# Kernel tuning notes

Measured on AMD Instinct MI355X. Metric: run time of the kernel, lower is better.

## Reference

```python
import jax, jax.numpy as jnp
import numpy as np
import math

B, S, D = 2, 2048, 2048
H, KV, HD = 32, 8, 64
G = H // KV  # 4
BASE = 10000.0


def _rope_tables(seq_len, dtype):
    inv_freq = 1.0 / (BASE ** (jnp.arange(0, HD, 2, dtype=jnp.float32) / HD))
    t = jnp.arange(seq_len, dtype=jnp.float32)
    freqs = jnp.outer(t, inv_freq)               # [S, HD/2]
    emb = jnp.concatenate([freqs, freqs], -1)     # [S, HD]
    return jnp.cos(emb).astype(dtype), jnp.sin(emb).astype(dtype)


def _rotate_half(x):
    x1, x2 = x[..., : HD // 2], x[..., HD // 2 :]
    return jnp.concatenate([-x2, x1], axis=-1)


def setup_inputs() -> dict:
    key = jax.random.key(0)
    ks = jax.random.split(key, 5)
    s = 0.02
    return {
        "hidden_states": jax.random.normal(ks[0], (B, S, D), jnp.float32),
        "Wq": jax.random.normal(ks[1], (D, H * HD), jnp.float32) * s,
        "Wk": jax.random.normal(ks[2], (D, KV * HD), jnp.float32) * s,
        "Wv": jax.random.normal(ks[3], (D, KV * HD), jnp.float32) * s,
        "Wo": jax.random.normal(ks[4], (D, D), jnp.float32) * s,
    }


def reference(hidden_states, Wq, Wk, Wv, Wo):
    b, s, _ = hidden_states.shape
    q = (hidden_states @ Wq).reshape(b, s, H, HD).transpose(0, 2, 1, 3)   # [B,H,S,HD]
    k = (hidden_states @ Wk).reshape(b, s, KV, HD).transpose(0, 2, 1, 3)  # [B,KV,S,HD]
    v = (hidden_states @ Wv).reshape(b, s, KV, HD).transpose(0, 2, 1, 3)

    cos, sin = _rope_tables(s, hidden_states.dtype)  # [S, HD]
    cos = cos[None, None]
    sin = sin[None, None]
    q = q * cos + _rotate_half(q) * sin
    k = k * cos + _rotate_half(k) * sin

    # GQA: repeat kv heads to match query heads
    k = jnp.repeat(k, G, axis=1)  # [B,H,S,HD]
    v = jnp.repeat(v, G, axis=1)

    scores = jnp.einsum("bhqd,bhkd->bhqk", q, k) / math.sqrt(HD)
    causal = jnp.triu(jnp.full((s, s), float("-inf"), dtype=scores.dtype), k=1)
    scores = scores + causal
    attn = jax.nn.softmax(scores, axis=-1)
    out = jnp.einsum("bhqk,bhkd->bhqd", attn, v)          # [B,H,S,HD]
    out = out.transpose(0, 2, 1, 3).reshape(b, s, H * HD)  # [B,S,D]
    return out @ Wo
```

## Files before the change

kernel.cpp:

```cpp
#include <hip/hip_runtime.h>
#include <hip/hip_bf16.h>

#define BATCH  2
#define SEQ    2048
#define DMODEL 2048
#define NHEADS 32
#define NKV    8
#define HDIM   64
#define ROWS   (BATCH * SEQ)
#define NQKV   3072

typedef __attribute__((ext_vector_type(8))) short bf16x8;
typedef __attribute__((ext_vector_type(4))) float floatx4;

__device__ __forceinline__ float b2f(unsigned short u) {
    union { unsigned int i; float f; } x; x.i = ((unsigned int)u) << 16; return x.f;
}
__device__ __forceinline__ unsigned short f2b(float f) {
    union { float f; unsigned int i; } x; x.f = f;
    unsigned int r = x.i + 0x7fffu + ((x.i >> 16) & 1u);
    return (unsigned short)(r >> 16);
}
__device__ __forceinline__ unsigned int pkbf(float a, float b) {
    union { __hip_bfloat162 h; unsigned int u; } x;
    x.h = __float22bfloat162_rn(make_float2(a, b));
    return x.u;
}

#define GLD16(g, l) __builtin_amdgcn_global_load_lds( \
    (const __attribute__((address_space(1))) unsigned int*)(g), \
    (__attribute__((address_space(3))) unsigned int*)(l), 16, 0, 0)

template <bool BF16_OUT>
__global__ __launch_bounds__(256) void mfma_gemm(const unsigned short* __restrict__ A,
                                                 const unsigned short* __restrict__ Bt,
                                                 void* __restrict__ Cout,
                                                 int M, int N, int K) {
    __shared__ unsigned short As[128 * 32];
    __shared__ unsigned short Bs[128 * 32];

    const int tid  = threadIdx.x;
    const int wave = tid >> 6;
    const int lane = tid & 63;
    const int m0 = blockIdx.y * 128;
    const int n0 = blockIdx.x * 128;
    const int wr0 = (wave >> 1) * 64;
    const int wc0 = (wave & 1) * 64;

    const int srow = wave * 32 + (lane >> 2);
    const int skc  = (lane & 3) * 8;
    const unsigned short* Ap0 = A  + (size_t)(m0 + srow) * K + skc;
    const unsigned short* Ap1 = Ap0 + (size_t)16 * K;
    const unsigned short* Bp0 = Bt + (size_t)(n0 + srow) * K + skc;
    const unsigned short* Bp1 = Bp0 + (size_t)16 * K;
    unsigned short* Al0 = &As[wave * 1024];
    unsigned short* Al1 = &As[wave * 1024 + 512];
    unsigned short* Bl0 = &Bs[wave * 1024];
    unsigned short* Bl1 = &Bs[wave * 1024 + 512];

    const int fr = lane & 15;
    const int fk = (lane >> 4) * 8;

    floatx4 acc[4][4];
    #pragma unroll
    for (int r = 0; r < 4; ++r)
        #pragma unroll
        for (int c = 0; c < 4; ++c)
            #pragma unroll
            for (int g = 0; g < 4; ++g) acc[r][c][g] = 0.f;

    for (int k0 = 0; k0 < K; k0 += 32) {
        __syncthreads();
        GLD16(Ap0 + k0, Al0);
        GLD16(Ap1 + k0, Al1);
        GLD16(Bp0 + k0, Bl0);
        GLD16(Bp1 + k0, Bl1);
        __syncthreads();

        bf16x8 af[4], bfr[4];
        #pragma unroll
        for (int r = 0; r < 4; ++r)
            af[r] = *(const bf16x8*)&As[(wr0 + r * 16 + fr) * 32 + fk];
        #pragma unroll
        for (int c = 0; c < 4; ++c)
            bfr[c] = *(const bf16x8*)&Bs[(wc0 + c * 16 + fr) * 32 + fk];
        #pragma unroll
        for (int r = 0; r < 4; ++r)
            #pragma unroll
            for (int c = 0; c < 4; ++c)
                acc[r][c] = __builtin_amdgcn_mfma_f32_16x16x32_bf16(af[r], bfr[c], acc[r][c], 0, 0, 0);
    }

    const int erow = (lane >> 4) * 4;
    const int ecol = lane & 15;
    #pragma unroll
    for (int r = 0; r < 4; ++r)
        #pragma unroll
        for (int c = 0; c < 4; ++c)
            #pragma unroll
            for (int g = 0; g < 4; ++g) {
                int row = m0 + wr0 + r * 16 + erow + g;
                int col = n0 + wc0 + c * 16 + ecol;
                if (BF16_OUT)
                    ((unsigned short*)Cout)[(size_t)row * N + col] = f2b(acc[r][c][g]);
                else
                    ((float*)Cout)[(size_t)row * N + col] = acc[r][c][g];
            }
}

__global__ __launch_bounds__(256) void transpose_cast_all(const float* __restrict__ Wq,
                                                          const float* __restrict__ Wk,
                                                          const float* __restrict__ Wv,
                                                          const float* __restrict__ Wo,
                                                          unsigned short* __restrict__ Wt,
                                                          unsigned short* __restrict__ Wot) {
    __shared__ float t[32][33];
    int bx = blockIdx.x;
    const float* src; unsigned short* dst; int N, nb;
    if (bx < 64)      { src = Wq; dst = Wt;                          N = 2048; nb = bx; }
    else if (bx < 80) { src = Wk; dst = Wt + (size_t)2048 * DMODEL;  N = 512;  nb = bx - 64; }
    else if (bx < 96) { src = Wv; dst = Wt + (size_t)2560 * DMODEL;  N = 512;  nb = bx - 80; }
    else              { src = Wo; dst = Wot;                         N = 2048; nb = bx - 96; }
    const int n0 = nb * 32, k0 = blockIdx.y * 32;
    const int tx = threadIdx.x & 31, ty = threadIdx.x >> 5;
    #pragma unroll
    for (int i = 0; i < 32; i += 8)
        t[ty + i][tx] = src[(size_t)(k0 + ty + i) * N + n0 + tx];
    __syncthreads();
    #pragma unroll
    for (int i = 0; i < 32; i += 8)
        dst[(size_t)(n0 + ty + i) * DMODEL + k0 + tx] = f2b(t[tx][ty + i]);
}

__global__ void cast_f32_to_bf16(const float* __restrict__ src,
                                 unsigned short* __restrict__ dst, int n) {
    int i = (blockIdx.x * 256 + threadIdx.x) * 8;
    if (i >= n) return;
    float4 a = *(const float4*)(src + i);
    float4 b = *(const float4*)(src + i + 4);
    uint4 o;
    o.x = pkbf(a.x, a.y); o.y = pkbf(a.z, a.w);
    o.z = pkbf(b.x, b.y); o.w = pkbf(b.z, b.w);
    *(uint4*)(dst + i) = o;
}

__global__ void rope_all(unsigned short* __restrict__ buf) {
    int idx = blockIdx.x * blockDim.x + threadIdx.x;
    int i   = idx & 31;
    int tmp = idx >> 5;
    int hh  = tmp % 40;
    int row = tmp / 40;
    if (row >= ROWS) return;
    float scale = (hh < 32) ? 0.125f : 1.0f;
    int t = row & (SEQ - 1);
    float inv_freq = powf(10000.0f, -(float)i * (1.0f / 32.0f));
    float ang = (float)t * inv_freq;
    float s, c;
    sincosf(ang, &s, &c);
    unsigned short* p = buf + (size_t)row * NQKV + hh * 64 + i;
    float x1 = b2f(p[0]), x2 = b2f(p[32]);
    p[0]  = f2b((x1 * c - x2 * s) * scale);
    p[32] = f2b((x2 * c + x1 * s) * scale);
}

__global__ __launch_bounds__(256, 5) void attn_mfma(const unsigned short* __restrict__ QKV,
                                                    unsigned short* __restrict__ Ctx) {
    __shared__ unsigned short Ks[64][72];
    __shared__ unsigned short Vts[64][72];
    __shared__ unsigned short Ps[4][16][72];

    const int tid  = threadIdx.x;
    const int wave = tid >> 6;
    const int lane = tid & 63;
    const int px = blockIdx.x;
    const int h  = blockIdx.y;
    const int b  = blockIdx.z;
    const int kvh = h >> 2;

    const int fr = lane & 15;
    const int fg = lane >> 4;
    const size_t base = (size_t)(b * SEQ) * NQKV;

    const int krow = tid >> 2, kc0 = (tid & 3) * 16;
    const int vp2 = tid & 31, vh0 = (tid >> 5) * 8;
    const unsigned short* kbase = QKV + base + (size_t)krow * NQKV + 2048 + kvh * HDIM + kc0;
    const unsigned short* vbase = QKV + base + (size_t)(2 * vp2) * NQKV + 2560 + kvh * HDIM + vh0;

    #pragma unroll 1
    for (int t = 0; t < 2; ++t) {
        const int qb = (t == 0) ? (31 - px) : px;
        const int wbase = qb * 64 + wave * 16;

        bf16x8 qf[2];
        #pragma unroll
        for (int ks = 0; ks < 2; ++ks)
            qf[ks] = *(const bf16x8*)(QKV + base + (size_t)(wbase + fr) * NQKV
                                      + h * HDIM + ks * 32 + fg * 8);

        float l = 0.f;
        floatx4 acc[4];
        #pragma unroll
        for (int j2 = 0; j2 < 4; ++j2)
            #pragma unroll
            for (int g = 0; g < 4; ++g) acc[j2][g] = 0.f;

        const int nkb = qb + 1;

        bf16x8 kr0 = *(const bf16x8*)kbase;
        bf16x8 kr1 = *(const bf16x8*)(kbase + 8);
        bf16x8 v0  = *(const bf16x8*)vbase;
        bf16x8 v1  = *(const bf16x8*)(vbase + NQKV);

        for (int kb = 0; kb < nkb; ++kb) {
            __syncthreads();
            *(bf16x8*)&Ks[krow][kc0]     = kr0;
            *(bf16x8*)&Ks[krow][kc0 + 8] = kr1;
            #pragma unroll
            for (int j = 0; j < 8; ++j) {
                unsigned int w = (unsigned int)(unsigned short)v0[j]
                               | ((unsigned int)(unsigned short)v1[j] << 16);
                *(unsigned int*)&Vts[vh0 + j][2 * vp2] = w;
            }
            {
                int nx = (kb + 1 < nkb) ? kb + 1 : kb;
                const unsigned short* kp = kbase + (size_t)(nx * 64) * NQKV;
                const unsigned short* vp = vbase + (size_t)(nx * 64) * NQKV;
                kr0 = *(const bf16x8*)kp;
                kr1 = *(const bf16x8*)(kp + 8);
                v0  = *(const bf16x8*)vp;
                v1  = *(const bf16x8*)(vp + NQKV);
            }
            __syncthreads();

            const bool skip = (kb * 64 > wbase + 15);
            if (!skip) {
                const bool needMask = (kb * 64 + 63 > wbase);

                floatx4 sc[4];
                #pragma unroll
                for (int j = 0; j < 4; ++j)
                    #pragma unroll
                    for (int g = 0; g < 4; ++g) sc[j][g] = 0.f;
                __builtin_amdgcn_s_setprio(1);
                #pragma unroll
                for (int ks = 0; ks < 2; ++ks) {
                    #pragma unroll
                    for (int j = 0; j < 4; ++j) {
                        bf16x8 kf = *(const bf16x8*)&Ks[j * 16 + fr][ks * 32 + fg * 8];
                        sc[j] = __builtin_amdgcn_mfma_f32_16x16x32_bf16(kf, qf[ks], sc[j], 0, 0, 0);
                    }
                }
                __builtin_amdgcn_s_setprio(0);

                if (needMask) {
                    int qi = wbase + fr;
                    #pragma unroll
                    for (int j = 0; j < 4; ++j)
                        #pragma unroll
                        for (int g = 0; g < 4; ++g) {
                            int kj = kb * 64 + j * 16 + fg * 4 + g;
                            if (kj > qi) sc[j][g] = -1e30f;
                        }
                }

                #pragma unroll
                for (int j = 0; j < 4; ++j) {
                    #pragma unroll
                    for (int g = 0; g < 4; ++g) {
                        float e = __expf(sc[j][g]);
                        sc[j][g] = e;
                        l += e;
                    }
                    uint2 w;
                    w.x = pkbf(sc[j][0], sc[j][1]);
                    w.y = pkbf(sc[j][2], sc[j][3]);
                    *(uint2*)&Ps[wave][fr][j * 16 + fg * 4] = w;
                }

                __builtin_amdgcn_s_setprio(1);
                #pragma unroll
                for (int ks = 0; ks < 2; ++ks) {
                    bf16x8 pf = *(const bf16x8*)&Ps[wave][fr][ks * 32 + fg * 8];
                    #pragma unroll
                    for (int j2 = 0; j2 < 4; ++j2) {
                        bf16x8 vf = *(const bf16x8*)&Vts[j2 * 16 + fr][ks * 32 + fg * 8];
                        acc[j2] = __builtin_amdgcn_mfma_f32_16x16x32_bf16(vf, pf, acc[j2], 0, 0, 0);
                    }
                }
                __builtin_amdgcn_s_setprio(0);
            }
        }

        {
            float lt = l;
            lt += __shfl_xor(lt, 16);
            lt += __shfl_xor(lt, 32);
            float inv = 1.0f / lt;
            int q = wbase + fr;
            unsigned short* cp = Ctx + (size_t)(b * SEQ + q) * DMODEL + h * HDIM;
            #pragma unroll
            for (int j2 = 0; j2 < 4; ++j2) {
                uint2 w;
                w.x = pkbf(acc[j2][0] * inv, acc[j2][1] * inv);
                w.y = pkbf(acc[j2][2] * inv, acc[j2][3] * inv);
                *(uint2*)(cp + j2 * 16 + fg * 4) = w;
            }
        }
    }
}

extern "C" void kernel_launch(void* const* d_in, const int* in_sizes, int n_in,
                              void* d_out, int out_size, void* d_ws, size_t ws_size,
                              hipStream_t stream) {
    const float* X  = (const float*)d_in[0];
    const float* Wq = (const float*)d_in[1];
    const float* Wk = (const float*)d_in[2];
    const float* Wv = (const float*)d_in[3];
    const float* Wo = (const float*)d_in[4];
    float* out = (float*)d_out;

    unsigned short* Xb   = (unsigned short*)d_ws;
    unsigned short* Wt   = Xb + (size_t)ROWS * DMODEL;
    unsigned short* Wot  = Wt + (size_t)NQKV * DMODEL;
    unsigned short* QKVb = Wot + (size_t)DMODEL * DMODEL;
    unsigned short* Ctxb = QKVb + (size_t)ROWS * NQKV;

    cast_f32_to_bf16<<<(ROWS * DMODEL) / (8 * 256), 256, 0, stream>>>(X, Xb, ROWS * DMODEL);
    transpose_cast_all<<<dim3(160, 64), 256, 0, stream>>>(Wq, Wk, Wv, Wo, Wt, Wot);

    mfma_gemm<true><<<dim3(NQKV / 128, ROWS / 128), 256, 0, stream>>>(Xb, Wt, QKVb, ROWS, NQKV, DMODEL);

    rope_all<<<(ROWS * 40 * 32) / 256, 256, 0, stream>>>(QKVb);

    attn_mfma<<<dim3(SEQ / 128, NHEADS, BATCH), 256, 0, stream>>>(QKVb, Ctxb);

    mfma_gemm<false><<<dim3(DMODEL / 128, ROWS / 128), 256, 0, stream>>>(Ctxb, Wot, out, ROWS, DMODEL, DMODEL);
}
```

Measured before the change: 329.8 us.

## Triple-buffer LDS tiles in MFMA GEMM to overlap global loads with compute

Replaces the single-buffered load-sync-compute loop in the bf16 MFMA GEMM with a three-stage LDS ring. Tiles are prefetched two iterations ahead using global_load_lds, and explicit vmcnt waits plus one barrier per iteration replace the two __syncthreads. This is meant to hide global memory latency behind MFMA work. It triples the LDS footprint, which may reduce occupancy, and it relies on hand-placed waitcnt counts being correct.

```diff
diff --git a/kernel.cpp b/kernel.cpp
--- a/kernel.cpp
+++ b/kernel.cpp
@@ -36,8 +36,8 @@
                                                  const unsigned short* __restrict__ Bt,
                                                  void* __restrict__ Cout,
                                                  int M, int N, int K) {
-    __shared__ unsigned short As[128 * 32];
-    __shared__ unsigned short Bs[128 * 32];
+    __shared__ unsigned short As[3][128 * 32];
+    __shared__ unsigned short Bs[3][128 * 32];
 
     const int tid  = threadIdx.x;
     const int wave = tid >> 6;
@@ -53,10 +53,6 @@
     const unsigned short* Ap1 = Ap0 + (size_t)16 * K;
     const unsigned short* Bp0 = Bt + (size_t)(n0 + srow) * K + skc;
     const unsigned short* Bp1 = Bp0 + (size_t)16 * K;
-    unsigned short* Al0 = &As[wave * 1024];
-    unsigned short* Al1 = &As[wave * 1024 + 512];
-    unsigned short* Bl0 = &Bs[wave * 1024];
-    unsigned short* Bl1 = &Bs[wave * 1024 + 512];
 
     const int fr = lane & 15;
     const int fk = (lane >> 4) * 8;
@@ -69,26 +65,53 @@
             #pragma unroll
             for (int g = 0; g < 4; ++g) acc[r][c][g] = 0.f;
 
-    for (int k0 = 0; k0 < K; k0 += 32) {
-        __syncthreads();
-        GLD16(Ap0 + k0, Al0);
-        GLD16(Ap1 + k0, Al1);
-        GLD16(Bp0 + k0, Bl0);
-        GLD16(Bp1 + k0, Bl1);
-        __syncthreads();
-
+    const int NT = K >> 5;
+
+    auto stage = [&](int t, int buf) {
+        unsigned short* Ab = &As[buf][wave * 1024];
+        unsigned short* Bb = &Bs[buf][wave * 1024];
+        const int k0 = t * 32;
+        GLD16(Ap0 + k0, Ab);
+        GLD16(Ap1 + k0, Ab + 512);
+        GLD16(Bp0 + k0, Bb);
+        GLD16(Bp1 + k0, Bb + 512);
+    };
+
+    stage(0, 0);
+    stage(1, 1);
+    asm volatile("s_waitcnt vmcnt(4)" ::: "memory");
+    __builtin_amdgcn_s_barrier();
+    __builtin_amdgcn_sched_barrier(0);
+
+    int cur = 0, nx2 = 2;
+    for (int T = 0; T < NT; ++T) {
+        if (T + 2 < NT) stage(T + 2, nx2);
+
+        const unsigned short* Asb = &As[cur][0];
+        const unsigned short* Bsb = &Bs[cur][0];
         bf16x8 af[4], bfr[4];
         #pragma unroll
         for (int r = 0; r < 4; ++r)
-            af[r] = *(const bf16x8*)&As[(wr0 + r * 16 + fr) * 32 + fk];
+            af[r] = *(const bf16x8*)&Asb[(wr0 + r * 16 + fr) * 32 + fk];
         #pragma unroll
         for (int c = 0; c < 4; ++c)
-            bfr[c] = *(const bf16x8*)&Bs[(wc0 + c * 16 + fr) * 32 + fk];
+            bfr[c] = *(const bf16x8*)&Bsb[(wc0 + c * 16 + fr) * 32 + fk];
         #pragma unroll
         for (int r = 0; r < 4; ++r)
             #pragma unroll
             for (int c = 0; c < 4; ++c)
                 acc[r][c] = __builtin_amdgcn_mfma_f32_16x16x32_bf16(af[r], bfr[c], acc[r][c], 0, 0, 0);
+
+        if (T + 1 < NT) {
+            if (T + 2 < NT)
+                asm volatile("s_waitcnt vmcnt(4)" ::: "memory");
+            else
+                asm volatile("s_waitcnt vmcnt(0)" ::: "memory");
+            __builtin_amdgcn_s_barrier();
+            __builtin_amdgcn_sched_barrier(0);
+        }
+        cur = (cur == 2) ? 0 : cur + 1;
+        nx2 = (nx2 == 2) ? 0 : nx2 + 1;
     }
 
     const int erow = (lane >> 4) * 4;
```

New measurement: 320.6 us. 1.03x faster.
